# Kernel optimization log

Hardware: AMD Instinct MI355X
Metric: run time of the kernel (lower is better)

## Reference

```python
import jax, jax.numpy as jnp
import numpy as np

B = 262144   # batch_size
DX = 4       # dim_x (state vector 4)
DIMS = [DX, 32, 32, 64, 64, DX]  # fc1, fc_add1, fc2, fc_add2, fc3


def _glorot(key, fan_in, fan_out):
    std = (2.0 / (fan_in + fan_out)) ** 0.5
    return jax.random.normal(key, (fan_in, fan_out), dtype=jnp.float32) * std


def setup_inputs() -> dict:
    key = jax.random.key(0)
    ks = jax.random.split(key, 6)
    inp = {}
    for i in range(5):
        inp[f"W{i+1}"] = _glorot(ks[i], DIMS[i], DIMS[i + 1])
        inp[f"b{i+1}"] = jnp.zeros((DIMS[i + 1],), dtype=jnp.float32)
    inp["last_state"] = jax.random.normal(ks[5], (B, 1, DX), dtype=jnp.float32)
    inp["training"] = 1
    return inp


def _mlp(x, W1, b1, W2, b2, W3, b3, W4, b4, W5, b5):
    # fc1 -> fc_add1 -> fc2 -> fc_add2 -> fc3 (last layer linear)
    h = jax.nn.relu(x @ W1 + b1)
    h = jax.nn.relu(h @ W2 + b2)
    h = jax.nn.relu(h @ W3 + b3)
    h = jax.nn.relu(h @ W4 + b4)
    return h @ W5 + b5


def reference(last_state, W1, b1, W2, b2, W3, b3, W4, b4, W5, b5, training):
    # new_state = last_state + MLP(last_state), shape [B, 1, DX]
    new_state = last_state + _mlp(last_state, W1, b1, W2, b2, W3, b3, W4, b4, W5, b5)

    # batch Jacobian F = d new_state / d last_state, reshaped to [B, DX, DX]
    xs = last_state[:, 0, :]  # [B, DX]

    def f(v):  # per-sample residual update, v: [DX]
        return v + _mlp(v, W1, b1, W2, b2, W3, b3, W4, b4, W5, b5)

    F = jax.vmap(jax.jacfwd(f))(xs)  # [B, DX, DX]; jacfwd is cheap: only DX=4 tangents
    return new_state, F
```

## Files before the change

### kernel.cpp

```cpp
#include <hip/hip_runtime.h>

typedef __attribute__((ext_vector_type(8))) short short8;
typedef __attribute__((ext_vector_type(4))) float f32x4;
typedef __attribute__((ext_vector_type(2))) float f32x2;
typedef __attribute__((ext_vector_type(2))) unsigned uint2v;

#define NWAVES 2
#define BLOCK (64 * NWAVES)
#define TB 8192
#define FWDB 8192
#define WBYTES (FWDB + 6 * 64 * 4)

__device__ __forceinline__ unsigned short f2bf(float f) {
    unsigned u = __builtin_bit_cast(unsigned, f);
    u += 0x7FFFu + ((u >> 16) & 1u);
    return (unsigned short)(u >> 16);
}

__device__ __forceinline__ int taddr(int row, int slot) {
    return row * 128 + (((slot ^ (row & 7)) << 4));
}

__device__ __forceinline__ f32x2 pkfma(f32x2 a, f32x2 b, f32x2 c) {
    return __builtin_elementwise_fma(a, b, c);
}

__device__ __forceinline__ short8 loadB(const float* __restrict__ W, int Nout, int Kin,
                                        int kbase, int col) {
    short8 r;
#pragma unroll
    for (int i = 0; i < 8; ++i) {
        int k = kbase + i;
        float v = (k < Kin && col < Nout) ? W[k * Nout + col] : 0.0f;
        r[i] = (short)f2bf(v);
    }
    return r;
}

template<int MT, int KT, int W0, int NW>
__device__ __forceinline__ void tan_layer_T(unsigned char* wb, const unsigned* mkS,
                                            const short8* Wf, int lane)
{
    const int G = lane >> 4, sl = lane & 15;
#pragma unroll
    for (int nt = 0; nt < 4; ++nt) {
        const int s = nt * 16 + sl;
        short8 bt[KT];
#pragma unroll
        for (int kt = 0; kt < KT; ++kt)
            bt[kt] = *(const short8*)(wb + taddr(s, 4 * kt + G));
        unsigned mwords[NW];
#pragma unroll
        for (int w = 0; w < NW; ++w) mwords[w] = mkS[s * 6 + W0 + w];
#pragma unroll
        for (int mt = 0; mt < MT; ++mt) {
            f32x4 c = {0.f, 0.f, 0.f, 0.f};
#pragma unroll
            for (int kt = 0; kt < KT; ++kt)
                c = __builtin_amdgcn_mfma_f32_16x16x32_bf16(Wf[kt * MT + mt], bt[kt], c, 0, 0, 0);
            const unsigned mw = mwords[(mt * 16) >> 5] >> ((mt & 1) * 16 + G * 4);
            const float v0 = (mw & 1u) ? c[0] : 0.0f;
            const float v1 = (mw & 2u) ? c[1] : 0.0f;
            const float v2 = (mw & 4u) ? c[2] : 0.0f;
            const float v3 = (mw & 8u) ? c[3] : 0.0f;
            unsigned lo, hi;
            asm("v_cvt_pk_bf16_f32 %0, %1, %2" : "=v"(lo) : "v"(v0), "v"(v1));
            asm("v_cvt_pk_bf16_f32 %0, %1, %2" : "=v"(hi) : "v"(v2), "v"(v3));
            const int slot = 2 * mt + (G >> 1);
            uint2v pk; pk[0] = lo; pk[1] = hi;
            *(uint2v*)(wb + s * 128 + ((slot ^ (s & 7)) << 4) + 8 * (G & 1)) = pk;
        }
    }
}

__device__ __forceinline__ void tan_final_T(unsigned char* wb, const short8* B5,
                                            int lane, int r,
                                            float* __restrict__ out_F, int sbase)
{
    const int G = lane >> 4, sl = lane & 15;
#pragma unroll
    for (int nt = 0; nt < 4; ++nt) {
        const int s = nt * 16 + sl;
        short8 b0 = *(const short8*)(wb + taddr(s, G));
        short8 b1 = *(const short8*)(wb + taddr(s, 4 + G));
        f32x4 c = {0.f, 0.f, 0.f, 0.f};
        c = __builtin_amdgcn_mfma_f32_16x16x32_bf16(B5[0], b0, c, 0, 0, 0);
        c = __builtin_amdgcn_mfma_f32_16x16x32_bf16(B5[1], b1, c, 0, 0, 0);
        if (G == 0) {
#pragma unroll
            for (int i = 0; i < 4; ++i)
                out_F[(size_t)(sbase + s) * 16 + i * 4 + r] = c[i] + ((i == r) ? 1.0f : 0.0f);
        }
    }
}

__global__ __launch_bounds__(BLOCK)
void mlp_jac_kernel(
    const float* __restrict__ W1, const float* __restrict__ b1,
    const float* __restrict__ W2, const float* __restrict__ b2,
    const float* __restrict__ W3, const float* __restrict__ b3,
    const float* __restrict__ W4, const float* __restrict__ b4,
    const float* __restrict__ W5, const float* __restrict__ b5,
    const float* __restrict__ xin,
    float* __restrict__ out_state, float* __restrict__ out_F, int Btot)
{
    __shared__ __align__(16) unsigned char smem[NWAVES][WBYTES];
    const int tid = threadIdx.x;
    const int wid = tid >> 6;
    const int lane = tid & 63;
    const int sbase = blockIdx.x * BLOCK + wid * 64;
    if (sbase >= Btot) return;

    unsigned char* wb = smem[wid];
    unsigned* mkS = (unsigned*)(wb + FWDB);

    const int s_my = sbase + lane;
    const float4 xv = *reinterpret_cast<const float4*>(xin + 4 * s_my);
    const float xa[4] = {xv.x, xv.y, xv.z, xv.w};

    unsigned m1, m2;
    unsigned long long m3, m4;
    {
        float acc[32];
#pragma unroll
        for (int j = 0; j < 32; ++j) {
            float a = b1[j];
#pragma unroll
            for (int k = 0; k < 4; ++k) a = fmaf(xa[k], W1[k * 32 + j], a);
            acc[j] = a;
        }
        unsigned m = 0;
#pragma unroll
        for (int j = 0; j < 32; ++j) {
            const bool p = acc[j] > 0.0f;
            m |= ((unsigned)(p ? 1 : 0)) << j;
            acc[j] = p ? acc[j] : 0.0f;
        }
#pragma unroll
        for (int jb = 0; jb < 8; ++jb) {
            float4 v; v.x = acc[4*jb]; v.y = acc[4*jb+1]; v.z = acc[4*jb+2]; v.w = acc[4*jb+3];
            *(float4*)(wb + taddr(lane, jb)) = v;
        }
        m1 = m;
    }
    {
        f32x2 acc[16];
#pragma unroll
        for (int j = 0; j < 16; ++j) { acc[j][0] = b2[2*j]; acc[j][1] = b2[2*j+1]; }
#pragma unroll 2
        for (int kb = 0; kb < 8; ++kb) {
            const float4 cv4 = *(const float4*)(wb + taddr(lane, kb));
            const float cvs[4] = {cv4.x, cv4.y, cv4.z, cv4.w};
#pragma unroll
            for (int ki = 0; ki < 4; ++ki) {
                const f32x2 cv = {cvs[ki], cvs[ki]};
                const int k = 4 * kb + ki;
#pragma unroll
                for (int j = 0; j < 16; ++j)
                    acc[j] = pkfma(cv, *(const f32x2*)(W2 + k * 32 + 2 * j), acc[j]);
            }
        }
        unsigned m = 0;
#pragma unroll
        for (int j = 0; j < 16; ++j) {
            const bool p0 = acc[j][0] > 0.0f, p1 = acc[j][1] > 0.0f;
            m |= ((unsigned)(p0 ? 1 : 0)) << (2*j);
            m |= ((unsigned)(p1 ? 1 : 0)) << (2*j+1);
            acc[j][0] = p0 ? acc[j][0] : 0.0f;
            acc[j][1] = p1 ? acc[j][1] : 0.0f;
        }
#pragma unroll
        for (int jb = 0; jb < 8; ++jb) {
            float4 v; v.x = acc[2*jb][0]; v.y = acc[2*jb][1]; v.z = acc[2*jb+1][0]; v.w = acc[2*jb+1][1];
            *(float4*)(wb + taddr(lane, jb)) = v;
        }
        m2 = m;
    }
    f32x2 h3r[16];
    {
        f32x2 acc[32];
#pragma unroll
        for (int j = 0; j < 32; ++j) { acc[j][0] = b3[2*j]; acc[j][1] = b3[2*j+1]; }
#pragma unroll 2
        for (int kb = 0; kb < 8; ++kb) {
            const float4 cv4 = *(const float4*)(wb + taddr(lane, kb));
            const float cvs[4] = {cv4.x, cv4.y, cv4.z, cv4.w};
#pragma unroll
            for (int ki = 0; ki < 4; ++ki) {
                const f32x2 cv = {cvs[ki], cvs[ki]};
                const int k = 4 * kb + ki;
#pragma unroll
                for (int j = 0; j < 32; ++j)
                    acc[j] = pkfma(cv, *(const f32x2*)(W3 + k * 64 + 2 * j), acc[j]);
            }
        }
        unsigned long long m = 0ULL;
#pragma unroll
        for (int j = 0; j < 32; ++j) {
            const bool p0 = acc[j][0] > 0.0f, p1 = acc[j][1] > 0.0f;
            m |= ((unsigned long long)(p0 ? 1 : 0)) << (2*j);
            m |= ((unsigned long long)(p1 ? 1 : 0)) << (2*j+1);
            acc[j][0] = p0 ? acc[j][0] : 0.0f;
            acc[j][1] = p1 ? acc[j][1] : 0.0f;
        }
#pragma unroll
        for (int jb = 0; jb < 8; ++jb) {
            float4 v; v.x = acc[2*jb][0]; v.y = acc[2*jb][1]; v.z = acc[2*jb+1][0]; v.w = acc[2*jb+1][1];
            *(float4*)(wb + taddr(lane, jb)) = v;
        }
#pragma unroll
        for (int t = 0; t < 16; ++t) h3r[t] = acc[16 + t];
        m3 = m;
    }
    {
        f32x2 acc[32];
#pragma unroll
        for (int j = 0; j < 32; ++j) { acc[j][0] = b4[2*j]; acc[j][1] = b4[2*j+1]; }
#pragma unroll 2
        for (int kb = 0; kb < 8; ++kb) {
            const float4 cv4 = *(const float4*)(wb + taddr(lane, kb));
            const float cvs[4] = {cv4.x, cv4.y, cv4.z, cv4.w};
#pragma unroll
            for (int ki = 0; ki < 4; ++ki) {
                const f32x2 cv = {cvs[ki], cvs[ki]};
                const int k = 4 * kb + ki;
#pragma unroll
                for (int j = 0; j < 32; ++j)
                    acc[j] = pkfma(cv, *(const f32x2*)(W4 + k * 64 + 2 * j), acc[j]);
            }
        }
#pragma unroll
        for (int t = 0; t < 32; ++t) {
            const float cs = h3r[t >> 1][t & 1];
            const f32x2 cv = {cs, cs};
#pragma unroll
            for (int j = 0; j < 32; ++j)
                acc[j] = pkfma(cv, *(const f32x2*)(W4 + (32 + t) * 64 + 2 * j), acc[j]);
        }
        unsigned long long m = 0ULL;
        f32x2 y01 = {b5[0], b5[1]}, y23 = {b5[2], b5[3]};
#pragma unroll
        for (int j = 0; j < 32; ++j) {
#pragma unroll
            for (int e = 0; e < 2; ++e) {
                const int u = 2 * j + e;
                const bool p = acc[j][e] > 0.0f;
                m |= ((unsigned long long)(p ? 1 : 0)) << u;
                const float hv = p ? acc[j][e] : 0.0f;
                const f32x2 hvv = {hv, hv};
                y01 = pkfma(hvv, *(const f32x2*)(W5 + u * 4), y01);
                y23 = pkfma(hvv, *(const f32x2*)(W5 + u * 4 + 2), y23);
            }
        }
        m4 = m;
        float4 o;
        o.x = xa[0] + y01[0]; o.y = xa[1] + y01[1];
        o.z = xa[2] + y23[0]; o.w = xa[3] + y23[1];
        *reinterpret_cast<float4*>(out_state + 4 * s_my) = o;
    }
    mkS[lane * 6 + 0] = m1;
    mkS[lane * 6 + 1] = m2;
    mkS[lane * 6 + 2] = (unsigned)(m3 & 0xffffffffULL);
    mkS[lane * 6 + 3] = (unsigned)(m3 >> 32);
    mkS[lane * 6 + 4] = (unsigned)(m4 & 0xffffffffULL);
    mkS[lane * 6 + 5] = (unsigned)(m4 >> 32);

    __builtin_amdgcn_sched_barrier(0);

    const int col = lane & 15, G = lane >> 4;
    short8 W2f[2], W3f[4], W4f[8], W5f[2];
#pragma unroll
    for (int mt = 0; mt < 2; ++mt) W2f[mt] = loadB(W2, 32, 32, 8 * G, 16 * mt + col);
#pragma unroll
    for (int mt = 0; mt < 4; ++mt) W3f[mt] = loadB(W3, 64, 32, 8 * G, 16 * mt + col);
#pragma unroll
    for (int kt = 0; kt < 2; ++kt)
#pragma unroll
        for (int mt = 0; mt < 4; ++mt)
            W4f[kt * 4 + mt] = loadB(W4, 64, 64, 32 * kt + 8 * G, 16 * mt + col);
#pragma unroll
    for (int kt = 0; kt < 2; ++kt) W5f[kt] = loadB(W5, 4, 64, 32 * kt + 8 * G, col);

    for (int r = 0; r < 4; ++r) {
#pragma unroll
        for (int sl = 0; sl < 4; ++sl) {
            short8 v;
#pragma unroll
            for (int e = 0; e < 8; ++e) {
                const int u = sl * 8 + e;
                v[e] = ((m1 >> u) & 1u) ? (short)f2bf(W1[r * 32 + u]) : (short)0;
            }
            *(short8*)(wb + taddr(lane, sl)) = v;
        }
        tan_layer_T<2, 1, 1, 1>(wb, mkS, W2f, lane);
        tan_layer_T<4, 1, 2, 2>(wb, mkS, W3f, lane);
        tan_layer_T<4, 2, 4, 2>(wb, mkS, W4f, lane);
        tan_final_T(wb, W5f, lane, r, out_F, sbase);
    }
}

extern "C" void kernel_launch(void* const* d_in, const int* in_sizes, int n_in,
                              void* d_out, int out_size, void* d_ws, size_t ws_size,
                              hipStream_t stream)
{
    const float* W1 = (const float*)d_in[0];
    const float* b1 = (const float*)d_in[1];
    const float* W2 = (const float*)d_in[2];
    const float* b2 = (const float*)d_in[3];
    const float* W3 = (const float*)d_in[4];
    const float* b3 = (const float*)d_in[5];
    const float* W4 = (const float*)d_in[6];
    const float* b4 = (const float*)d_in[7];
    const float* W5 = (const float*)d_in[8];
    const float* b5 = (const float*)d_in[9];
    const float* xin = (const float*)d_in[10];

    const int Btot = in_sizes[10] / 4;
    float* out_state = (float*)d_out;
    float* out_F = out_state + (size_t)Btot * 4;

    const int grid = (Btot + BLOCK - 1) / BLOCK;
    mlp_jac_kernel<<<grid, BLOCK, 0, stream>>>(
        W1, b1, W2, b2, W3, b3, W4, b4, W5, b5, xin, out_state, out_F, Btot);
}
```

Baseline: 102.0 us.

## Split fused kernel into forward and tangent kernels with masks in workspace

Splits the single fused kernel into a forward kernel that computes the state and ReLU masks, and a tangent kernel that reads those masks from a global workspace and runs the MFMA Jacobian pass. Each kernel has a smaller register and shared-memory footprint, which may allow higher occupancy. In exchange it adds a second launch and a global write and read of 24 bytes of mask per sample.

Result: slower. 129.9 us (+27.3%).

```diff
diff --git a/kernel.cpp b/kernel.cpp
--- a/kernel.cpp
+++ b/kernel.cpp
@@ -9,7 +9,6 @@
 #define BLOCK (64 * NWAVES)
 #define TB 8192
 #define FWDB 8192
-#define WBYTES (FWDB + 6 * 64 * 4)
 
 __device__ __forceinline__ unsigned short f2bf(float f) {
     unsigned u = __builtin_bit_cast(unsigned, f);
@@ -35,6 +34,177 @@
         r[i] = (short)f2bf(v);
     }
     return r;
+}
+
+__global__ __launch_bounds__(BLOCK)
+void fwd_kernel(
+    const float* __restrict__ W1, const float* __restrict__ b1,
+    const float* __restrict__ W2, const float* __restrict__ b2,
+    const float* __restrict__ W3, const float* __restrict__ b3,
+    const float* __restrict__ W4, const float* __restrict__ b4,
+    const float* __restrict__ W5, const float* __restrict__ b5,
+    const float* __restrict__ xin,
+    float* __restrict__ out_state, unsigned* __restrict__ maskG, int Btot)
+{
+    __shared__ __align__(16) unsigned char smem[NWAVES][FWDB];
+    const int tid = threadIdx.x;
+    const int wid = tid >> 6;
+    const int lane = tid & 63;
+    const int sbase = blockIdx.x * BLOCK + wid * 64;
+    if (sbase >= Btot) return;
+
+    unsigned char* wb = smem[wid];
+    const int s_my = sbase + lane;
+    const float4 xv = *reinterpret_cast<const float4*>(xin + 4 * s_my);
+    const float xa[4] = {xv.x, xv.y, xv.z, xv.w};
+
+    unsigned m1, m2;
+    unsigned long long m3, m4;
+    {
+        float acc[32];
+#pragma unroll
+        for (int j = 0; j < 32; ++j) {
+            float a = b1[j];
+#pragma unroll
+            for (int k = 0; k < 4; ++k) a = fmaf(xa[k], W1[k * 32 + j], a);
+            acc[j] = a;
+        }
+        unsigned m = 0;
+#pragma unroll
+        for (int j = 0; j < 32; ++j) {
+            const bool p = acc[j] > 0.0f;
+            m |= ((unsigned)(p ? 1 : 0)) << j;
+            acc[j] = p ? acc[j] : 0.0f;
+        }
+#pragma unroll
+        for (int jb = 0; jb < 8; ++jb) {
+            float4 v; v.x = acc[4*jb]; v.y = acc[4*jb+1]; v.z = acc[4*jb+2]; v.w = acc[4*jb+3];
+            *(float4*)(wb + taddr(lane, jb)) = v;
+        }
+        m1 = m;
+    }
+    {
+        f32x2 acc[16];
+#pragma unroll
+        for (int j = 0; j < 16; ++j) { acc[j][0] = b2[2*j]; acc[j][1] = b2[2*j+1]; }
+#pragma unroll 2
+        for (int kb = 0; kb < 8; ++kb) {
+            const float4 cv4 = *(const float4*)(wb + taddr(lane, kb));
+            const float cvs[4] = {cv4.x, cv4.y, cv4.z, cv4.w};
+#pragma unroll
+            for (int ki = 0; ki < 4; ++ki) {
+                const f32x2 cv = {cvs[ki], cvs[ki]};
+                const int k = 4 * kb + ki;
+#pragma unroll
+                for (int j = 0; j < 16; ++j)
+                    acc[j] = pkfma(cv, *(const f32x2*)(W2 + k * 32 + 2 * j), acc[j]);
+            }
+        }
+        unsigned m = 0;
+#pragma unroll
+        for (int j = 0; j < 16; ++j) {
+            const bool p0 = acc[j][0] > 0.0f, p1 = acc[j][1] > 0.0f;
+            m |= ((unsigned)(p0 ? 1 : 0)) << (2*j);
+            m |= ((unsigned)(p1 ? 1 : 0)) << (2*j+1);
+            acc[j][0] = p0 ? acc[j][0] : 0.0f;
+            acc[j][1] = p1 ? acc[j][1] : 0.0f;
+        }
+#pragma unroll
+        for (int jb = 0; jb < 8; ++jb) {
+            float4 v; v.x = acc[2*jb][0]; v.y = acc[2*jb][1]; v.z = acc[2*jb+1][0]; v.w = acc[2*jb+1][1];
+            *(float4*)(wb + taddr(lane, jb)) = v;
+        }
+        m2 = m;
+    }
+    f32x2 h3r[16];
+    {
+        f32x2 acc[32];
+#pragma unroll
+        for (int j = 0; j < 32; ++j) { acc[j][0] = b3[2*j]; acc[j][1] = b3[2*j+1]; }
+#pragma unroll 2
+        for (int kb = 0; kb < 8; ++kb) {
+            const float4 cv4 = *(const float4*)(wb + taddr(lane, kb));
+            const float cvs[4] = {cv4.x, cv4.y, cv4.z, cv4.w};
+#pragma unroll
+            for (int ki = 0; ki < 4; ++ki) {
+                const f32x2 cv = {cvs[ki], cvs[ki]};
+                const int k = 4 * kb + ki;
+#pragma unroll
+                for (int j = 0; j < 32; ++j)
+                    acc[j] = pkfma(cv, *(const f32x2*)(W3 + k * 64 + 2 * j), acc[j]);
+            }
+        }
+        unsigned long long m = 0ULL;
+#pragma unroll
+        for (int j = 0; j < 32; ++j) {
+            const bool p0 = acc[j][0] > 0.0f, p1 = acc[j][1] > 0.0f;
+            m |= ((unsigned long long)(p0 ? 1 : 0)) << (2*j);
+            m |= ((unsigned long long)(p1 ? 1 : 0)) << (2*j+1);
+            acc[j][0] = p0 ? acc[j][0] : 0.0f;
+            acc[j][1] = p1 ? acc[j][1] : 0.0f;
+        }
+#pragma unroll
+        for (int jb = 0; jb < 8; ++jb) {
+            float4 v; v.x = acc[2*jb][0]; v.y = acc[2*jb][1]; v.z = acc[2*jb+1][0]; v.w = acc[2*jb+1][1];
+            *(float4*)(wb + taddr(lane, jb)) = v;
+        }
+#pragma unroll
+        for (int t = 0; t < 16; ++t) h3r[t] = acc[16 + t];
+        m3 = m;
+    }
+    {
+        f32x2 acc[32];
+#pragma unroll
+        for (int j = 0; j < 32; ++j) { acc[j][0] = b4[2*j]; acc[j][1] = b4[2*j+1]; }
+#pragma unroll 2
+        for (int kb = 0; kb < 8; ++kb) {
+            const float4 cv4 = *(const float4*)(wb + taddr(lane, kb));
+            const float cvs[4] = {cv4.x, cv4.y, cv4.z, cv4.w};
+#pragma unroll
+            for (int ki = 0; ki < 4; ++ki) {
+                const f32x2 cv = {cvs[ki], cvs[ki]};
+                const int k = 4 * kb + ki;
+#pragma unroll
+                for (int j = 0; j < 32; ++j)
+                    acc[j] = pkfma(cv, *(const f32x2*)(W4 + k * 64 + 2 * j), acc[j]);
+            }
+        }
+#pragma unroll
+        for (int t = 0; t < 32; ++t) {
+            const float cs = h3r[t >> 1][t & 1];
+            const f32x2 cv = {cs, cs};
+#pragma unroll
+            for (int j = 0; j < 32; ++j)
+                acc[j] = pkfma(cv, *(const f32x2*)(W4 + (32 + t) * 64 + 2 * j), acc[j]);
+        }
+        unsigned long long m = 0ULL;
+        f32x2 y01 = {b5[0], b5[1]}, y23 = {b5[2], b5[3]};
+#pragma unroll
+        for (int j = 0; j < 32; ++j) {
+#pragma unroll
+            for (int e = 0; e < 2; ++e) {
+                const int u = 2 * j + e;
+                const bool p = acc[j][e] > 0.0f;
+                m |= ((unsigned long long)(p ? 1 : 0)) << u;
+                const float hv = p ? acc[j][e] : 0.0f;
+                const f32x2 hvv = {hv, hv};
+                y01 = pkfma(hvv, *(const f32x2*)(W5 + u * 4), y01);
+                y23 = pkfma(hvv, *(const f32x2*)(W5 + u * 4 + 2), y23);
+            }
+        }
+        m4 = m;
+        float4 o;
+        o.x = xa[0] + y01[0]; o.y = xa[1] + y01[1];
+        o.z = xa[2] + y23[0]; o.w = xa[3] + y23[1];
+        *reinterpret_cast<float4*>(out_state + 4 * s_my) = o;
+    }
+    unsigned* mg = maskG + (size_t)s_my * 6;
+    mg[0] = m1;
+    mg[1] = m2;
+    mg[2] = (unsigned)(m3 & 0xffffffffULL);
+    mg[3] = (unsigned)(m3 >> 32);
+    mg[4] = (unsigned)(m4 & 0xffffffffULL);
+    mg[5] = (unsigned)(m4 >> 32);
 }
 
 template<int MT, int KT, int W0, int NW>
@@ -95,16 +265,14 @@
 }
 
 __global__ __launch_bounds__(BLOCK)
-void mlp_jac_kernel(
-    const float* __restrict__ W1, const float* __restrict__ b1,
-    const float* __restrict__ W2, const float* __restrict__ b2,
-    const float* __restrict__ W3, const float* __restrict__ b3,
-    const float* __restrict__ W4, const float* __restrict__ b4,
-    const float* __restrict__ W5, const float* __restrict__ b5,
-    const float* __restrict__ xin,
-    float* __restrict__ out_state, float* __restrict__ out_F, int Btot)
-{
-    __shared__ __align__(16) unsigned char smem[NWAVES][WBYTES];
+void tan_kernel(
+    const float* __restrict__ W1, const float* __restrict__ W2,
+    const float* __restrict__ W3, const float* __restrict__ W4,
+    const float* __restrict__ W5,
+    const unsigned* __restrict__ maskG,
+    float* __restrict__ out_F, int Btot)
+{
+    __shared__ __align__(16) unsigned char smem[NWAVES][TB + 6 * 64 * 4];
     const int tid = threadIdx.x;
     const int wid = tid >> 6;
     const int lane = tid & 63;
@@ -112,160 +280,16 @@
     if (sbase >= Btot) return;
 
     unsigned char* wb = smem[wid];
-    unsigned* mkS = (unsigned*)(wb + FWDB);
-
-    const int s_my = sbase + lane;
-    const float4 xv = *reinterpret_cast<const float4*>(xin + 4 * s_my);
-    const float xa[4] = {xv.x, xv.y, xv.z, xv.w};
-
-    unsigned m1, m2;
-    unsigned long long m3, m4;
-    {
-        float acc[32];
-#pragma unroll
-        for (int j = 0; j < 32; ++j) {
-            float a = b1[j];
-#pragma unroll
-            for (int k = 0; k < 4; ++k) a = fmaf(xa[k], W1[k * 32 + j], a);
-            acc[j] = a;
-        }
-        unsigned m = 0;
-#pragma unroll
-        for (int j = 0; j < 32; ++j) {
-            const bool p = acc[j] > 0.0f;
-            m |= ((unsigned)(p ? 1 : 0)) << j;
-            acc[j] = p ? acc[j] : 0.0f;
-        }
-#pragma unroll
-        for (int jb = 0; jb < 8; ++jb) {
-            float4 v; v.x = acc[4*jb]; v.y = acc[4*jb+1]; v.z = acc[4*jb+2]; v.w = acc[4*jb+3];
-            *(float4*)(wb + taddr(lane, jb)) = v;
-        }
-        m1 = m;
-    }
-    {
-        f32x2 acc[16];
-#pragma unroll
-        for (int j = 0; j < 16; ++j) { acc[j][0] = b2[2*j]; acc[j][1] = b2[2*j+1]; }
-#pragma unroll 2
-        for (int kb = 0; kb < 8; ++kb) {
-            const float4 cv4 = *(const float4*)(wb + taddr(lane, kb));
-            const float cvs[4] = {cv4.x, cv4.y, cv4.z, cv4.w};
-#pragma unroll
-            for (int ki = 0; ki < 4; ++ki) {
-                const f32x2 cv = {cvs[ki], cvs[ki]};
-                const int k = 4 * kb + ki;
-#pragma unroll
-                for (int j = 0; j < 16; ++j)
-                    acc[j] = pkfma(cv, *(const f32x2*)(W2 + k * 32 + 2 * j), acc[j]);
-            }
-        }
-        unsigned m = 0;
-#pragma unroll
-        for (int j = 0; j < 16; ++j) {
-            const bool p0 = acc[j][0] > 0.0f, p1 = acc[j][1] > 0.0f;
-            m |= ((unsigned)(p0 ? 1 : 0)) << (2*j);
-            m |= ((unsigned)(p1 ? 1 : 0)) << (2*j+1);
-            acc[j][0] = p0 ? acc[j][0] : 0.0f;
-            acc[j][1] = p1 ? acc[j][1] : 0.0f;
-        }
-#pragma unroll
-        for (int jb = 0; jb < 8; ++jb) {
-            float4 v; v.x = acc[2*jb][0]; v.y = acc[2*jb][1]; v.z = acc[2*jb+1][0]; v.w = acc[2*jb+1][1];
-            *(float4*)(wb + taddr(lane, jb)) = v;
-        }
-        m2 = m;
-    }
-    f32x2 h3r[16];
-    {
-        f32x2 acc[32];
-#pragma unroll
-        for (int j = 0; j < 32; ++j) { acc[j][0] = b3[2*j]; acc[j][1] = b3[2*j+1]; }
-#pragma unroll 2
-        for (int kb = 0; kb < 8; ++kb) {
-            const float4 cv4 = *(const float4*)(wb + taddr(lane, kb));
-            const float cvs[4] = {cv4.x, cv4.y, cv4.z, cv4.w};
-#pragma unroll
-            for (int ki = 0; ki < 4; ++ki) {
-                const f32x2 cv = {cvs[ki], cvs[ki]};
-                const int k = 4 * kb + ki;
-#pragma unroll
-                for (int j = 0; j < 32; ++j)
-                    acc[j] = pkfma(cv, *(const f32x2*)(W3 + k * 64 + 2 * j), acc[j]);
-            }
-        }
-        unsigned long long m = 0ULL;
-#pragma unroll
-        for (int j = 0; j < 32; ++j) {
-            const bool p0 = acc[j][0] > 0.0f, p1 = acc[j][1] > 0.0f;
-            m |= ((unsigned long long)(p0 ? 1 : 0)) << (2*j);
-            m |= ((unsigned long long)(p1 ? 1 : 0)) << (2*j+1);
-            acc[j][0] = p0 ? acc[j][0] : 0.0f;
-            acc[j][1] = p1 ? acc[j][1] : 0.0f;
-        }
-#pragma unroll
-        for (int jb = 0; jb < 8; ++jb) {
-            float4 v; v.x = acc[2*jb][0]; v.y = acc[2*jb][1]; v.z = acc[2*jb+1][0]; v.w = acc[2*jb+1][1];
-            *(float4*)(wb + taddr(lane, jb)) = v;
-        }
-#pragma unroll
-        for (int t = 0; t < 16; ++t) h3r[t] = acc[16 + t];
-        m3 = m;
-    }
-    {
-        f32x2 acc[32];
-#pragma unroll
-        for (int j = 0; j < 32; ++j) { acc[j][0] = b4[2*j]; acc[j][1] = b4[2*j+1]; }
-#pragma unroll 2
-        for (int kb = 0; kb < 8; ++kb) {
-            const float4 cv4 = *(const float4*)(wb + taddr(lane, kb));
-            const float cvs[4] = {cv4.x, cv4.y, cv4.z, cv4.w};
-#pragma unroll
-            for (int ki = 0; ki < 4; ++ki) {
-                const f32x2 cv = {cvs[ki], cvs[ki]};
-                const int k = 4 * kb + ki;
-#pragma unroll
-                for (int j = 0; j < 32; ++j)
-                    acc[j] = pkfma(cv, *(const f32x2*)(W4 + k * 64 + 2 * j), acc[j]);
-            }
-        }
-#pragma unroll
-        for (int t = 0; t < 32; ++t) {
-            const float cs = h3r[t >> 1][t & 1];
-            const f32x2 cv = {cs, cs};
-#pragma unroll
-            for (int j = 0; j < 32; ++j)
-                acc[j] = pkfma(cv, *(const f32x2*)(W4 + (32 + t) * 64 + 2 * j), acc[j]);
-        }
-        unsigned long long m = 0ULL;
-        f32x2 y01 = {b5[0], b5[1]}, y23 = {b5[2], b5[3]};
-#pragma unroll
-        for (int j = 0; j < 32; ++j) {
-#pragma unroll
-            for (int e = 0; e < 2; ++e) {
-                const int u = 2 * j + e;
-                const bool p = acc[j][e] > 0.0f;
-                m |= ((unsigned long long)(p ? 1 : 0)) << u;
-                const float hv = p ? acc[j][e] : 0.0f;
-                const f32x2 hvv = {hv, hv};
-                y01 = pkfma(hvv, *(const f32x2*)(W5 + u * 4), y01);
-                y23 = pkfma(hvv, *(const f32x2*)(W5 + u * 4 + 2), y23);
-            }
-        }
-        m4 = m;
-        float4 o;
-        o.x = xa[0] + y01[0]; o.y = xa[1] + y01[1];
-        o.z = xa[2] + y23[0]; o.w = xa[3] + y23[1];
-        *reinterpret_cast<float4*>(out_state + 4 * s_my) = o;
-    }
-    mkS[lane * 6 + 0] = m1;
-    mkS[lane * 6 + 1] = m2;
-    mkS[lane * 6 + 2] = (unsigned)(m3 & 0xffffffffULL);
-    mkS[lane * 6 + 3] = (unsigned)(m3 >> 32);
-    mkS[lane * 6 + 4] = (unsigned)(m4 & 0xffffffffULL);
-    mkS[lane * 6 + 5] = (unsigned)(m4 >> 32);
-
-    __builtin_amdgcn_sched_barrier(0);
+    unsigned* mkS = (unsigned*)(wb + TB);
+
+    const unsigned* mg = maskG + (size_t)(sbase + lane) * 6;
+    unsigned m1;
+    {
+        unsigned w0 = mg[0], w1 = mg[1], w2 = mg[2], w3 = mg[3], w4 = mg[4], w5 = mg[5];
+        m1 = w0;
+        unsigned* d = mkS + lane * 6;
+        d[0] = w0; d[1] = w1; d[2] = w2; d[3] = w3; d[4] = w4; d[5] = w5;
+    }
 
     const int col = lane & 15, G = lane >> 4;
     short8 W2f[2], W3f[4], W4f[8], W5f[2];
@@ -318,8 +342,11 @@
     const int Btot = in_sizes[10] / 4;
     float* out_state = (float*)d_out;
     float* out_F = out_state + (size_t)Btot * 4;
+    unsigned* maskG = (unsigned*)d_ws;
 
     const int grid = (Btot + BLOCK - 1) / BLOCK;
-    mlp_jac_kernel<<<grid, BLOCK, 0, stream>>>(
-        W1, b1, W2, b2, W3, b3, W4, b4, W5, b5, xin, out_state, out_F, Btot);
-}
+    fwd_kernel<<<grid, BLOCK, 0, stream>>>(
+        W1, b1, W2, b2, W3, b3, W4, b4, W5, b5, xin, out_state, maskG, Btot);
+    tan_kernel<<<grid, BLOCK, 0, stream>>>(
+        W1, W2, W3, W4, W5, maskG, out_F, Btot);
+}
```
